# Optimization experiments

Measured on AMD Instinct MI355X. Metric: run time of the kernel, lower is better.

Reference implementation:

```python
import jax, jax.numpy as jnp
import numpy as np

E = 1024   # embed_dim
H = 1024   # hidden_dim
NH = 16    # num_heads
HD = H // NH
B, P, C = 2, 1024, 1024


def _layernorm(x, g, b):
    m = jnp.mean(x, axis=-1, keepdims=True)
    v = jnp.mean((x - m) ** 2, axis=-1, keepdims=True)
    return (x - m) / jnp.sqrt(v + 1e-5) * g + b


def _attention(problem, context, Wq, bq, Wk, bk, Wv, bv, mask, num_heads, head_dim, head_out_dim):
    # Faithful to source: head axis LAST in the reshape, mask added AFTER softmax.
    batch = problem.shape[0]
    q = (problem @ Wq + bq).reshape(batch, -1, head_dim, num_heads)      # b i d h
    k = (context @ Wk + bk).reshape(batch, -1, head_dim, num_heads)      # b j d h
    v = (context @ Wv + bv).reshape(batch, -1, head_out_dim, num_heads)  # b j o h
    scores = jnp.einsum('bidh,bjdh->bijh', q, k) / jnp.sqrt(jnp.asarray(head_dim, q.dtype))
    p = jax.nn.softmax(scores, axis=2)
    if mask is not None:
        p = p + mask[..., None]
    out = jnp.einsum('bijh,bjoh->bioh', p, v)
    return out.reshape(batch, -1, head_out_dim * num_heads)


def setup_inputs() -> dict:
    key = jax.random.key(0)
    ks = jax.random.split(key, 20)
    s = 0.02
    inp = {
        'x': jax.random.normal(ks[0], (B, P, E), jnp.float32),
        'context': jax.random.normal(ks[1], (B, C, E), jnp.float32),
        'causal_mask': jnp.zeros((B, P, P), jnp.float32),
        'problem_pad_mask': jnp.zeros((B, P, P), jnp.float32),
        'context_pad_mask': jnp.zeros((B, P, C), jnp.float32),
        # self-attn params (out_dim = E)
        'sa_Wq': jax.random.normal(ks[2], (E, H), jnp.float32) * s, 'sa_bq': jnp.zeros((H,), jnp.float32),
        'sa_Wk': jax.random.normal(ks[3], (E, H), jnp.float32) * s, 'sa_bk': jnp.zeros((H,), jnp.float32),
        'sa_Wv': jax.random.normal(ks[4], (E, E), jnp.float32) * s, 'sa_bv': jnp.zeros((E,), jnp.float32),
        # cross-attn params
        'ca_Wq': jax.random.normal(ks[5], (E, H), jnp.float32) * s, 'ca_bq': jnp.zeros((H,), jnp.float32),
        'ca_Wk': jax.random.normal(ks[6], (E, H), jnp.float32) * s, 'ca_bk': jnp.zeros((H,), jnp.float32),
        'ca_Wv': jax.random.normal(ks[7], (E, E), jnp.float32) * s, 'ca_bv': jnp.zeros((E,), jnp.float32),
        # layernorms
        'ln1_g': jnp.ones((E,), jnp.float32), 'ln1_b': jnp.zeros((E,), jnp.float32),
        'ln2_g': jnp.ones((E,), jnp.float32), 'ln2_b': jnp.zeros((E,), jnp.float32),
        'ln3_g': jnp.ones((E,), jnp.float32), 'ln3_b': jnp.zeros((E,), jnp.float32),
        # mlp
        'mlp_W1': jax.random.normal(ks[8], (E, H), jnp.float32) * s, 'mlp_b1': jnp.zeros((H,), jnp.float32),
        'mlp_W2': jax.random.normal(ks[9], (H, E), jnp.float32) * s, 'mlp_b2': jnp.zeros((E,), jnp.float32),
    }
    return inp


def reference(x, context, causal_mask, problem_pad_mask, context_pad_mask,
              sa_Wq, sa_bq, sa_Wk, sa_bk, sa_Wv, sa_bv,
              ca_Wq, ca_bq, ca_Wk, ca_bk, ca_Wv, ca_bv,
              ln1_g, ln1_b, ln2_g, ln2_b, ln3_g, ln3_b,
              mlp_W1, mlp_b1, mlp_W2, mlp_b2):
    self_attn_mask = causal_mask + problem_pad_mask
    xc = x
    x = _attention(x, x, sa_Wq, sa_bq, sa_Wk, sa_bk, sa_Wv, sa_bv, self_attn_mask, NH, HD, E // NH)
    x = _layernorm(x, ln1_g, ln1_b) + xc
    xc = x
    x = _attention(x, context, ca_Wq, ca_bq, ca_Wk, ca_bk, ca_Wv, ca_bv, context_pad_mask, NH, HD, E // NH)
    x = _layernorm(x, ln2_g, ln2_b) + xc
    xc = x
    x = jax.nn.relu(x @ mlp_W1 + mlp_b1) @ mlp_W2 + mlp_b2
    return _layernorm(x, ln3_g, ln3_b) + xc
```

## Files before the change

### kernel.cpp

```cpp
#include <hip/hip_runtime.h>
#include <math.h>

#define NHEADS 16

typedef __attribute__((ext_vector_type(8))) short bf16x8;
typedef __attribute__((ext_vector_type(4))) float f32x4;

__device__ inline short f2b(float f) {
  unsigned u = __float_as_uint(f);
  u += 0x7fffu + ((u >> 16) & 1u);
  return (short)(u >> 16);
}
__device__ inline float b2f(short s) {
  return __uint_as_float(((unsigned)(unsigned short)s) << 16);
}
__device__ inline void gld16(const void* g, void* l) {
  __builtin_amdgcn_global_load_lds(
      (const __attribute__((address_space(1))) unsigned int*)g,
      (__attribute__((address_space(3))) unsigned int*)l, 16, 0, 0);
}
#define MFMA16(a, b, c) __builtin_amdgcn_mfma_f32_16x16x32_bf16(a, b, c, 0, 0, 0)

__global__ __launch_bounds__(256) void prep_all(
    const float* __restrict__ x, const float* __restrict__ ctx,
    const float* __restrict__ cm, const float* __restrict__ ppm,
    const float* __restrict__ cpm,
    const float* sabq, const float* sabk, const float* sabv,
    const float* cabk, const float* cabv, const float* cabq,
    short* __restrict__ XB, short* __restrict__ CTXB,
    short* __restrict__ MBSA, short* __restrict__ MBCA,
    float* __restrict__ qkvb, float* __restrict__ kvb,
    float* __restrict__ qpb, unsigned* __restrict__ kmaxu) {
  const int blk = blockIdx.x;
  const int t = threadIdx.x;
  const int n4 = 2048 * 1024 / 4;
  if (blk < 8192) {
    int seg = blk >> 11;
    int i = (blk & 2047) * 256 + t;
    if (i >= n4) return;
    float4 va;
    short* out;
    if (seg == 0) { va = ((const float4*)x)[i]; out = XB; }
    else if (seg == 1) { va = ((const float4*)ctx)[i]; out = CTXB; }
    else if (seg == 2) {
      va = ((const float4*)cm)[i];
      float4 vb = ((const float4*)ppm)[i];
      va.x += vb.x; va.y += vb.y; va.z += vb.z; va.w += vb.w;
      out = MBSA;
    } else { va = ((const float4*)cpm)[i]; out = MBCA; }
    short4 s;
    s.x = f2b(va.x); s.y = f2b(va.y); s.z = f2b(va.z); s.w = f2b(va.w);
    ((short4*)out)[i] = s;
  } else {
    if (blk == 8192 && t < 64) kmaxu[t] = 0u;
    int i = (blk - 8192) * 256 + t;
    if (i >= 6144) return;
    int j = i & 1023;
    int pj = ((j & 63) << 4) | (j >> 6);
    int sec = i >> 10;
    if (sec == 0) qkvb[j] = sabq[pj];
    else if (sec == 1) qkvb[1024 + j] = sabk[pj];
    else if (sec == 2) qkvb[2048 + j] = sabv[pj];
    else if (sec == 3) kvb[j] = cabk[pj];
    else if (sec == 4) kvb[1024 + j] = cabv[pj];
    else qpb[j] = cabq[pj];
  }
}

__global__ __launch_bounds__(256) void wtrans(
    const float* W0, const float* W1, const float* W2, const float* W3,
    const float* W4, const float* W5, const float* W6, const float* W7,
    short* __restrict__ out) {
  __shared__ float t[64][65];
  const float* W;
  switch (blockIdx.z) {
    case 0: W = W0; break; case 1: W = W1; break;
    case 2: W = W2; break; case 3: W = W3; break;
    case 4: W = W4; break; case 5: W = W5; break;
    case 6: W = W6; break; default: W = W7; break;
  }
  const int permute = (blockIdx.z < 6) ? 1 : 0;
  short* o = out + (size_t)blockIdx.z * 1024 * 1024;
  const int tid = threadIdx.x;
  const int n0 = blockIdx.x * 64, k0 = blockIdx.y * 64;
  const int cg = (tid & 15) * 4, rg = tid >> 4;
  #pragma unroll
  for (int r = 0; r < 4; ++r) {
    int kl = rg + r * 16;
    float4 v = *(const float4*)(W + (size_t)(k0 + kl) * 1024 + n0 + cg);
    t[kl][cg + 0] = v.x; t[kl][cg + 1] = v.y;
    t[kl][cg + 2] = v.z; t[kl][cg + 3] = v.w;
  }
  __syncthreads();
  #pragma unroll
  for (int r = 0; r < 4; ++r) {
    int nl = rg + r * 16;
    int n = n0 + nl;
    int nrow = permute ? (((n & 15) << 6) | (n >> 4)) : n;
    short4 s;
    s.x = f2b(t[cg + 0][nl]); s.y = f2b(t[cg + 1][nl]);
    s.z = f2b(t[cg + 2][nl]); s.w = f2b(t[cg + 3][nl]);
    *(short4*)(o + (size_t)nrow * 1024 + k0 + cg) = s;
  }
}

__global__ __launch_bounds__(256) void knorm(const short* __restrict__ kh,
                                             unsigned* __restrict__ kmax) {
  const int bh = blockIdx.x, part = blockIdx.y;
  const int tid = threadIdx.x;
  const short* base = kh + (size_t)bh * 65536 +
                      (size_t)(part * 128 + (tid >> 1)) * 64 + (tid & 1) * 32;
  const bf16x8* rp = (const bf16x8*)base;
  float ssq = 0.f;
  #pragma unroll
  for (int c = 0; c < 4; ++c) {
    bf16x8 v = rp[c];
    #pragma unroll
    for (int e = 0; e < 8; ++e) { float f = b2f(v[e]); ssq += f * f; }
  }
  ssq += __shfl_xor(ssq, 1, 64);
  float mx = ssq;
  #pragma unroll
  for (int off = 2; off < 64; off <<= 1) mx = fmaxf(mx, __shfl_xor(mx, off, 64));
  __shared__ float wm[4];
  if ((tid & 63) == 0) wm[tid >> 6] = mx;
  __syncthreads();
  if (tid == 0)
    atomicMax(kmax + bh,
              __float_as_uint(fmaxf(fmaxf(wm[0], wm[1]), fmaxf(wm[2], wm[3]))));
}

__global__ __launch_bounds__(256) void gemm128(
    const short* __restrict__ A, const short* __restrict__ Bt,
    const float* __restrict__ bias,
    void* __restrict__ C0, short* __restrict__ C1, short* __restrict__ C2,
    int mode, int relu, int ny,
    const short* __restrict__ A2, const short* __restrict__ Bt2,
    const float* __restrict__ bias2,
    void* __restrict__ D0, short* __restrict__ D1, short* __restrict__ D2,
    int mode2, int relu2, int ny2) {
  if (blockIdx.z == 1) {
    A = A2; Bt = Bt2; bias = bias2;
    C0 = D0; C1 = D1; C2 = D2; mode = mode2; relu = relu2; ny = ny2;
  }
  if ((int)blockIdx.y >= ny) return;

  __shared__ short As[128 * 32];
  __shared__ short Bs[128 * 32];
  const int tid = threadIdx.x;
  const int w = tid >> 6, l = tid & 63;
  const int ln = l & 15, lq = l >> 4;
  const int wm = w >> 1, wn = w & 1;
  const int m0 = blockIdx.x * 128, n0 = blockIdx.y * 128;
  const int K = 1024;

  f32x4 acc[4][4];
  #pragma unroll
  for (int s = 0; s < 4; ++s)
    #pragma unroll
    for (int t = 0; t < 4; ++t) acc[s][t] = (f32x4){0.f, 0.f, 0.f, 0.f};

  const short* ga = A + (size_t)(m0 + w * 32 + (l >> 2)) * K + (l & 3) * 8;
  const short* gb = Bt + (size_t)(n0 + w * 32 + (l >> 2)) * K + (l & 3) * 8;
  short* lasA = &As[w * 1024];
  short* lasB = &Bs[w * 1024];

  for (int k0 = 0; k0 < K; k0 += 32) {
    __syncthreads();
    gld16(ga + k0, lasA);
    gld16(ga + (size_t)16 * K + k0, lasA + 512);
    gld16(gb + k0, lasB);
    gld16(gb + (size_t)16 * K + k0, lasB + 512);
    __syncthreads();
    bf16x8 af[4], bf[4];
    #pragma unroll
    for (int s = 0; s < 4; ++s)
      af[s] = *(const bf16x8*)&As[(wm * 64 + s * 16 + ln) * 32 + lq * 8];
    #pragma unroll
    for (int t = 0; t < 4; ++t)
      bf[t] = *(const bf16x8*)&Bs[(wn * 64 + t * 16 + ln) * 32 + lq * 8];
    #pragma unroll
    for (int s = 0; s < 4; ++s)
      #pragma unroll
      for (int t = 0; t < 4; ++t)
        acc[s][t] = MFMA16(af[s], bf[t], acc[s][t]);
  }

  float bv[4];
  #pragma unroll
  for (int t = 0; t < 4; ++t) bv[t] = bias[n0 + wn * 64 + t * 16 + ln];

  #pragma unroll
  for (int s = 0; s < 4; ++s) {
    #pragma unroll
    for (int t = 0; t < 4; ++t) {
      #pragma unroll
      for (int r = 0; r < 4; ++r) {
        int m = m0 + wm * 64 + s * 16 + lq * 4 + r;
        int n = n0 + wn * 64 + t * 16 + ln;
        float v = acc[s][t][r] + bv[t];
        if (relu) v = fmaxf(v, 0.f);
        int bb = m >> 10, ii = m & 1023;
        if (mode == 0) {
          ((float*)C0)[(size_t)m * 1024 + n] = v;
        } else if (mode == 1) {
          ((short*)C0)[(size_t)m * 1024 + n] = f2b(v);
        } else if (mode == 2) {
          int hh = n >> 6, d = n & 63;
          ((short*)C0)[(((size_t)(bb * 16 + hh)) * 1024 + ii) * 64 + d] = f2b(v);
        } else if (mode == 3) {
          int sel = n >> 10, g = n & 1023;
          int hh = g >> 6, d = g & 63;
          if (sel == 0)
            ((short*)C0)[(((size_t)(bb * 16 + hh)) * 1024 + ii) * 64 + d] = f2b(v);
          else if (sel == 1)
            C1[(((size_t)(bb * 16 + hh)) * 1024 + ii) * 64 + d] = f2b(v);
          else
            C2[(((size_t)(bb * 16 + hh)) * 64 + d) * 1024 + ii] = f2b(v);
        } else {
          int sel = n >> 10, g = n & 1023;
          int hh = g >> 6, d = g & 63;
          if (sel == 0)
            C1[(((size_t)(bb * 16 + hh)) * 1024 + ii) * 64 + d] = f2b(v);
          else
            C2[(((size_t)(bb * 16 + hh)) * 64 + d) * 1024 + ii] = f2b(v);
        }
      }
    }
  }
}

__global__ __launch_bounds__(256) void attn_flash(
    const short* __restrict__ qh, const short* __restrict__ kh,
    const short* __restrict__ vt, const short* __restrict__ maskb,
    const unsigned* __restrict__ kmax, float* __restrict__ out) {
  __shared__ short Ks[64 * 64];
  __shared__ short Vs[64 * 64];
  __shared__ short Msk[64 * 64];
  __shared__ short Ps[4][16 * 72];
  __shared__ float Ml[64];
  const int tid = threadIdx.x;
  const int w = tid >> 6, l = tid & 63;
  const int ln = l & 15, lq = l >> 4;
  const int it = blockIdx.x, h = blockIdx.y, b = blockIdx.z;
  const int i0 = it * 64;
  const int bh = b * 16 + h;
  const size_t bho = (size_t)bh * 65536;

  const short* qp = qh + bho + (size_t)(i0 + w * 16 + ln) * 64 + lq * 8;
  bf16x8 qf0 = *(const bf16x8*)qp;
  bf16x8 qf1 = *(const bf16x8*)(qp + 32);

  float ssq = 0.f;
  #pragma unroll
  for (int e = 0; e < 8; ++e) {
    float f0 = b2f(qf0[e]), f1 = b2f(qf1[e]);
    ssq += f0 * f0 + f1 * f1;
  }
  ssq += __shfl_xor(ssq, 16, 64);
  ssq += __shfl_xor(ssq, 32, 64);
  float km = sqrtf(__uint_as_float(kmax[bh])) * 1.0001f;
  if (lq == 0) Ml[w * 16 + ln] = sqrtf(ssq) * km * 0.125f + 1e-3f;
  float Mr[4], lac[4];
  #pragma unroll
  for (int r = 0; r < 4; ++r) { Mr[r] = Ml[w * 16 + lq * 4 + r]; lac[r] = 0.f; }

  const int srow = l >> 3;
  const int sch = (l & 7) ^ (srow & 7);
  const short* gk = kh + bho + (size_t)(w * 16 + srow) * 64 + sch * 8;
  const short* gv = vt + bho + (size_t)(w * 16 + srow) * 1024 + sch * 8;
  const short* gm = maskb + ((size_t)(b * 1024 + i0 + w * 16 + srow)) * 1024 + sch * 8;
  short* lk = &Ks[w * 1024];
  short* lv = &Vs[w * 1024];
  short* lm = &Msk[w * 1024];
  short* PsW = &Ps[w][0];

  f32x4 oa[4], mo[4];
  #pragma unroll
  for (int os = 0; os < 4; ++os) {
    oa[os] = (f32x4){0.f, 0.f, 0.f, 0.f};
    mo[os] = (f32x4){0.f, 0.f, 0.f, 0.f};
  }

  const int c0 = (lq ^ (ln & 7)) * 8;
  const int c1 = ((4 | lq) ^ (ln & 7)) * 8;

  for (int jt = 0; jt < 16; ++jt) {
    __syncthreads();
    gld16(gk + (size_t)jt * 4096, lk);
    gld16(gk + (size_t)jt * 4096 + 512, lk + 512);
    gld16(gv + (size_t)jt * 64, lv);
    gld16(gv + (size_t)jt * 64 + 8192, lv + 512);
    gld16(gm + (size_t)jt * 64, lm);
    gld16(gm + (size_t)jt * 64 + 8192, lm + 512);
    __syncthreads();

    f32x4 sa[4];
    #pragma unroll
    for (int js = 0; js < 4; ++js) {
      const short* kr = &Ks[(js * 16 + ln) * 64];
      bf16x8 kb0 = *(const bf16x8*)(kr + c0);
      bf16x8 kb1 = *(const bf16x8*)(kr + c1);
      f32x4 s = (f32x4){0.f, 0.f, 0.f, 0.f};
      s = MFMA16(qf0, kb0, s);
      s = MFMA16(qf1, kb1, s);
      sa[js] = s;
    }
    #pragma unroll
    for (int js = 0; js < 4; ++js)
      #pragma unroll
      for (int r = 0; r < 4; ++r) {
        float p = __expf(sa[js][r] * 0.125f - Mr[r]);
        lac[r] += p;
        PsW[(lq * 4 + r) * 72 + js * 16 + ln] = f2b(p);
      }
    bf16x8 pa0 = *(const bf16x8*)&PsW[ln * 72 + lq * 8];
    bf16x8 pa1 = *(const bf16x8*)&PsW[ln * 72 + 32 + lq * 8];
    const short* mr = &Msk[(w * 16 + ln) * 64];
    bf16x8 ma0 = *(const bf16x8*)(mr + c0);
    bf16x8 ma1 = *(const bf16x8*)(mr + c1);
    #pragma unroll
    for (int os = 0; os < 4; ++os) {
      const short* vr = &Vs[(os * 16 + ln) * 64];
      bf16x8 vb0 = *(const bf16x8*)(vr + c0);
      bf16x8 vb1 = *(const bf16x8*)(vr + c1);
      oa[os] = MFMA16(pa0, vb0, oa[os]);
      oa[os] = MFMA16(pa1, vb1, oa[os]);
      mo[os] = MFMA16(ma0, vb0, mo[os]);
      mo[os] = MFMA16(ma1, vb1, mo[os]);
    }
  }

  #pragma unroll
  for (int r = 0; r < 4; ++r) {
    lac[r] += __shfl_xor(lac[r], 1, 64);
    lac[r] += __shfl_xor(lac[r], 2, 64);
    lac[r] += __shfl_xor(lac[r], 4, 64);
    lac[r] += __shfl_xor(lac[r], 8, 64);
  }
  float inv[4];
  #pragma unroll
  for (int r = 0; r < 4; ++r) inv[r] = 1.f / lac[r];

  #pragma unroll
  for (int os = 0; os < 4; ++os)
    #pragma unroll
    for (int r = 0; r < 4; ++r) {
      int row = i0 + w * 16 + lq * 4 + r;
      int o = os * 16 + ln;
      out[bho + (size_t)row * 64 + o] = oa[os][r] * inv[r] + mo[os][r];
    }
}

__global__ __launch_bounds__(256) void ln_kernel(
    const float* __restrict__ x, const short* __restrict__ res,
    const float* __restrict__ g, const float* __restrict__ be,
    void* __restrict__ outp, int out_bf16, int inmode) {
  const int row = blockIdx.x;
  const int tid = threadIdx.x;
  float4 v;
  if (inmode == 0) {
    v = ((const float4*)(x + (size_t)row * 1024))[tid];
  } else {
    int b = row >> 10, i = row & 1023;
    const float* base = x + (size_t)b * 16 * 65536 + (size_t)i * 64;
    int o = tid >> 2, h0 = (tid & 3) * 4;
    v.x = base[(size_t)(h0 + 0) * 65536 + o];
    v.y = base[(size_t)(h0 + 1) * 65536 + o];
    v.z = base[(size_t)(h0 + 2) * 65536 + o];
    v.w = base[(size_t)(h0 + 3) * 65536 + o];
  }
  float s = v.x + v.y + v.z + v.w;
  float sq = v.x * v.x + v.y * v.y + v.z * v.z + v.w * v.w;
  #pragma unroll
  for (int off = 32; off > 0; off >>= 1) {
    s += __shfl_down(s, off, 64);
    sq += __shfl_down(sq, off, 64);
  }
  __shared__ float rs[4], rq[4], stat[2];
  int wave = tid >> 6, lane = tid & 63;
  if (lane == 0) { rs[wave] = s; rq[wave] = sq; }
  __syncthreads();
  if (tid == 0) {
    float S = rs[0] + rs[1] + rs[2] + rs[3];
    float Q = rq[0] + rq[1] + rq[2] + rq[3];
    float mean = S * (1.f / 1024.f);
    float var = Q * (1.f / 1024.f) - mean * mean;
    stat[0] = mean;
    stat[1] = rsqrtf(var + 1e-5f);
  }
  __syncthreads();
  float mean = stat[0], rstd = stat[1];
  float4 g4 = ((const float4*)g)[tid];
  float4 b4 = ((const float4*)be)[tid];
  short4 r4 = ((const short4*)(res + (size_t)row * 1024))[tid];
  float o0 = (v.x - mean) * rstd * g4.x + b4.x + b2f(r4.x);
  float o1 = (v.y - mean) * rstd * g4.y + b4.y + b2f(r4.y);
  float o2 = (v.z - mean) * rstd * g4.z + b4.z + b2f(r4.z);
  float o3 = (v.w - mean) * rstd * g4.w + b4.w + b2f(r4.w);
  if (out_bf16) {
    short4 o;
    o.x = f2b(o0); o.y = f2b(o1); o.z = f2b(o2); o.w = f2b(o3);
    ((short4*)outp)[(size_t)row * 256 + tid] = o;
  } else {
    float4 o = {o0, o1, o2, o3};
    ((float4*)outp)[(size_t)row * 256 + tid] = o;
  }
}

extern "C" void kernel_launch(void* const* d_in, const int* in_sizes, int n_in,
                              void* d_out, int out_size, void* d_ws, size_t ws_size,
                              hipStream_t stream) {
  const float* x    = (const float*)d_in[0];
  const float* ctx  = (const float*)d_in[1];
  const float* cm   = (const float*)d_in[2];
  const float* ppm  = (const float*)d_in[3];
  const float* cpm  = (const float*)d_in[4];
  const float* saWq = (const float*)d_in[5];
  const float* sabq = (const float*)d_in[6];
  const float* saWk = (const float*)d_in[7];
  const float* sabk = (const float*)d_in[8];
  const float* saWv = (const float*)d_in[9];
  const float* sabv = (const float*)d_in[10];
  const float* caWq = (const float*)d_in[11];
  const float* cabq = (const float*)d_in[12];
  const float* caWk = (const float*)d_in[13];
  const float* cabk = (const float*)d_in[14];
  const float* caWv = (const float*)d_in[15];
  const float* cabv = (const float*)d_in[16];
  const float* ln1g = (const float*)d_in[17];
  const float* ln1b = (const float*)d_in[18];
  const float* ln2g = (const float*)d_in[19];
  const float* ln2b = (const float*)d_in[20];
  const float* ln3g = (const float*)d_in[21];
  const float* ln3b = (const float*)d_in[22];
  const float* W1   = (const float*)d_in[23];
  const float* b1   = (const float*)d_in[24];
  const float* W2   = (const float*)d_in[25];
  const float* b2   = (const float*)d_in[26];

  char* ws = (char*)d_ws;
  const size_t MB = 1024 * 1024;
  short* WT       = (short*)(ws);
  float* qkvb     = (float*)(ws + 16 * MB);
  float* kvb      = (float*)(ws + 16 * MB + 16384);
  float* qpb      = (float*)(ws + 16 * MB + 32768);
  unsigned* kmaxu = (unsigned*)(ws + 16 * MB + 49152);
  short* MBSA  = (short*)(ws + 17 * MB);
  short* MBCA  = (short*)(ws + 21 * MB);
  short* XB    = (short*)(ws + 25 * MB);
  short* CTXB  = (short*)(ws + 29 * MB);
  short* QH    = (short*)(ws + 33 * MB);
  short* KH    = (short*)(ws + 37 * MB);
  short* VT    = (short*)(ws + 41 * MB);
  float* S3    = (float*)(ws + 45 * MB);
  short* X1B   = (short*)(ws + 53 * MB);
  short* X2B   = MBSA;
  short* HB    = CTXB;
  float* outp  = (float*)d_out;

  dim3 lg(2048);
  const short* dsp = nullptr;
  const float* dfp = nullptr;

  wtrans<<<dim3(16, 16, 8), 256, 0, stream>>>(saWq, saWk, saWv, caWk, caWv,
                                              caWq, W1, W2, WT);
  prep_all<<<dim3(8216), 256, 0, stream>>>(x, ctx, cm, ppm, cpm,
                                           sabq, sabk, sabv, cabk, cabv, cabq,
                                           XB, CTXB, MBSA, MBCA, qkvb, kvb, qpb,
                                           kmaxu);

  gemm128<<<dim3(16, 24, 1), 256, 0, stream>>>(
      XB, WT, qkvb, QH, KH, VT, 3, 0, 24,
      dsp, dsp, dfp, nullptr, nullptr, nullptr, 0, 0, 0);
  knorm<<<dim3(32, 8), 256, 0, stream>>>(KH, kmaxu);
  attn_flash<<<dim3(16, 16, 2), 256, 0, stream>>>(QH, KH, VT, MBSA, kmaxu, S3);
  ln_kernel<<<lg, 256, 0, stream>>>(S3, XB, ln1g, ln1b, X1B, 1, 1);

  gemm128<<<dim3(16, 16, 2), 256, 0, stream>>>(
      X1B, WT + 5 * 1048576, qpb, QH, nullptr, nullptr, 2, 0, 8,
      CTXB, WT + 3 * 1048576, kvb, nullptr, KH, VT, 4, 0, 16);
  knorm<<<dim3(32, 8), 256, 0, stream>>>(KH, kmaxu + 32);
  attn_flash<<<dim3(16, 16, 2), 256, 0, stream>>>(QH, KH, VT, MBCA, kmaxu + 32, S3);
  ln_kernel<<<lg, 256, 0, stream>>>(S3, X1B, ln2g, ln2b, X2B, 1, 1);

  gemm128<<<dim3(16, 8, 1), 256, 0, stream>>>(
      X2B, WT + 6 * 1048576, b1, HB, nullptr, nullptr, 1, 1, 8,
      dsp, dsp, dfp, nullptr, nullptr, nullptr, 0, 0, 0);
  gemm128<<<dim3(16, 8, 1), 256, 0, stream>>>(
      HB, WT + 7 * 1048576, b2, S3, nullptr, nullptr, 0, 0, 8,
      dsp, dsp, dfp, nullptr, nullptr, nullptr, 0, 0, 0);
  ln_kernel<<<lg, 256, 0, stream>>>(S3, X2B, ln3g, ln3b, outp, 0, 0);
}
```

Baseline: 350.0 us.

## Retile GEMMs to 64-row blocks with K=64 steps and XOR-swizzled LDS

Replaces the fixed 128x128 GEMM with a templated kernel that uses 64-row M tiles, a configurable N tile (128 or 64), and a K step of 64. LDS chunks are XOR-swizzled to avoid bank conflicts. Grids grow so that more blocks fill the CUs, since the old 16x8 grids used only 128 blocks for the MLP GEMMs. In exchange each block reuses less data, so global and LDS traffic per FLOP goes up.

```diff
diff --git a/kernel.cpp b/kernel.cpp
--- a/kernel.cpp
+++ b/kernel.cpp
@@ -130,7 +130,8 @@
               __float_as_uint(fmaxf(fmaxf(wm[0], wm[1]), fmaxf(wm[2], wm[3]))));
 }
 
-__global__ __launch_bounds__(256) void gemm128(
+template <int TN>
+__global__ __launch_bounds__(256) void gemmT(
     const short* __restrict__ A, const short* __restrict__ Bt,
     const float* __restrict__ bias,
     void* __restrict__ C0, short* __restrict__ C1, short* __restrict__ C2,
@@ -145,59 +146,67 @@
   }
   if ((int)blockIdx.y >= ny) return;
 
-  __shared__ short As[128 * 32];
-  __shared__ short Bs[128 * 32];
+  constexpr int NT = TN / 32;
+  constexpr int BR = TN / 4;
+  __shared__ short As[64 * 64];
+  __shared__ short Bs[TN * 64];
   const int tid = threadIdx.x;
   const int w = tid >> 6, l = tid & 63;
   const int ln = l & 15, lq = l >> 4;
   const int wm = w >> 1, wn = w & 1;
-  const int m0 = blockIdx.x * 128, n0 = blockIdx.y * 128;
+  const int m0 = blockIdx.x * 64, n0 = blockIdx.y * TN;
   const int K = 1024;
 
-  f32x4 acc[4][4];
-  #pragma unroll
-  for (int s = 0; s < 4; ++s)
-    #pragma unroll
-    for (int t = 0; t < 4; ++t) acc[s][t] = (f32x4){0.f, 0.f, 0.f, 0.f};
-
-  const short* ga = A + (size_t)(m0 + w * 32 + (l >> 2)) * K + (l & 3) * 8;
-  const short* gb = Bt + (size_t)(n0 + w * 32 + (l >> 2)) * K + (l & 3) * 8;
-  short* lasA = &As[w * 1024];
-  short* lasB = &Bs[w * 1024];
-
-  for (int k0 = 0; k0 < K; k0 += 32) {
+  f32x4 acc[2][NT];
+  #pragma unroll
+  for (int s = 0; s < 2; ++s)
+    #pragma unroll
+    for (int t = 0; t < NT; ++t) acc[s][t] = (f32x4){0.f, 0.f, 0.f, 0.f};
+
+  const int srow = l >> 3;
+  const int sch = (l & 7) ^ srow;
+  const short* ga = A + (size_t)(m0 + w * 16 + srow) * K + sch * 8;
+  const short* gb = Bt + (size_t)(n0 + w * BR + srow) * K + sch * 8;
+  short* la = &As[w * 16 * 64];
+  short* lb = &Bs[w * BR * 64];
+
+  for (int k0 = 0; k0 < K; k0 += 64) {
     __syncthreads();
-    gld16(ga + k0, lasA);
-    gld16(ga + (size_t)16 * K + k0, lasA + 512);
-    gld16(gb + k0, lasB);
-    gld16(gb + (size_t)16 * K + k0, lasB + 512);
+    gld16(ga + k0, la);
+    gld16(ga + (size_t)8 * K + k0, la + 512);
+    #pragma unroll
+    for (int rb = 0; rb < BR / 8; ++rb)
+      gld16(gb + (size_t)rb * 8 * K + k0, lb + rb * 512);
     __syncthreads();
-    bf16x8 af[4], bf[4];
-    #pragma unroll
-    for (int s = 0; s < 4; ++s)
-      af[s] = *(const bf16x8*)&As[(wm * 64 + s * 16 + ln) * 32 + lq * 8];
-    #pragma unroll
-    for (int t = 0; t < 4; ++t)
-      bf[t] = *(const bf16x8*)&Bs[(wn * 64 + t * 16 + ln) * 32 + lq * 8];
-    #pragma unroll
-    for (int s = 0; s < 4; ++s)
+    #pragma unroll
+    for (int kc = 0; kc < 2; ++kc) {
+      const int co = ((kc * 4 + lq) ^ (ln & 7)) * 8;
+      bf16x8 af[2], bf[NT];
+      af[0] = *(const bf16x8*)&As[(wm * 32 + ln) * 64 + co];
+      af[1] = *(const bf16x8*)&As[(wm * 32 + 16 + ln) * 64 + co];
       #pragma unroll
-      for (int t = 0; t < 4; ++t)
-        acc[s][t] = MFMA16(af[s], bf[t], acc[s][t]);
-  }
-
-  float bv[4];
-  #pragma unroll
-  for (int t = 0; t < 4; ++t) bv[t] = bias[n0 + wn * 64 + t * 16 + ln];
-
-  #pragma unroll
-  for (int s = 0; s < 4; ++s) {
-    #pragma unroll
-    for (int t = 0; t < 4; ++t) {
+      for (int t = 0; t < NT; ++t)
+        bf[t] = *(const bf16x8*)&Bs[(wn * (TN / 2) + t * 16 + ln) * 64 + co];
+      #pragma unroll
+      for (int s = 0; s < 2; ++s)
+        #pragma unroll
+        for (int t = 0; t < NT; ++t)
+          acc[s][t] = MFMA16(af[s], bf[t], acc[s][t]);
+    }
+  }
+
+  float bv[NT];
+  #pragma unroll
+  for (int t = 0; t < NT; ++t) bv[t] = bias[n0 + wn * (TN / 2) + t * 16 + ln];
+
+  #pragma unroll
+  for (int s = 0; s < 2; ++s) {
+    #pragma unroll
+    for (int t = 0; t < NT; ++t) {
       #pragma unroll
       for (int r = 0; r < 4; ++r) {
-        int m = m0 + wm * 64 + s * 16 + lq * 4 + r;
-        int n = n0 + wn * 64 + t * 16 + ln;
+        int m = m0 + wm * 32 + s * 16 + lq * 4 + r;
+        int n = n0 + wn * (TN / 2) + t * 16 + ln;
         float v = acc[s][t][r] + bv[t];
         if (relu) v = fmaxf(v, 0.f);
         int bb = m >> 10, ii = m & 1023;
@@ -470,25 +479,25 @@
                                            XB, CTXB, MBSA, MBCA, qkvb, kvb, qpb,
                                            kmaxu);
 
-  gemm128<<<dim3(16, 24, 1), 256, 0, stream>>>(
+  gemmT<128><<<dim3(32, 24, 1), 256, 0, stream>>>(
       XB, WT, qkvb, QH, KH, VT, 3, 0, 24,
       dsp, dsp, dfp, nullptr, nullptr, nullptr, 0, 0, 0);
   knorm<<<dim3(32, 8), 256, 0, stream>>>(KH, kmaxu);
   attn_flash<<<dim3(16, 16, 2), 256, 0, stream>>>(QH, KH, VT, MBSA, kmaxu, S3);
   ln_kernel<<<lg, 256, 0, stream>>>(S3, XB, ln1g, ln1b, X1B, 1, 1);
 
-  gemm128<<<dim3(16, 16, 2), 256, 0, stream>>>(
+  gemmT<128><<<dim3(32, 16, 2), 256, 0, stream>>>(
       X1B, WT + 5 * 1048576, qpb, QH, nullptr, nullptr, 2, 0, 8,
       CTXB, WT + 3 * 1048576, kvb, nullptr, KH, VT, 4, 0, 16);
   knorm<<<dim3(32, 8), 256, 0, stream>>>(KH, kmaxu + 32);
   attn_flash<<<dim3(16, 16, 2), 256, 0, stream>>>(QH, KH, VT, MBCA, kmaxu + 32, S3);
   ln_kernel<<<lg, 256, 0, stream>>>(S3, X1B, ln2g, ln2b, X2B, 1, 1);
 
-  gemm128<<<dim3(16, 8, 1), 256, 0, stream>>>(
-      X2B, WT + 6 * 1048576, b1, HB, nullptr, nullptr, 1, 1, 8,
+  gemmT<64><<<dim3(32, 16, 1), 256, 0, stream>>>(
+      X2B, WT + 6 * 1048576, b1, HB, nullptr, nullptr, 1, 1, 16,
       dsp, dsp, dfp, nullptr, nullptr, nullptr, 0, 0, 0);
-  gemm128<<<dim3(16, 8, 1), 256, 0, stream>>>(
-      HB, WT + 7 * 1048576, b2, S3, nullptr, nullptr, 0, 0, 8,
+  gemmT<64><<<dim3(32, 16, 1), 256, 0, stream>>>(
+      HB, WT + 7 * 1048576, b2, S3, nullptr, nullptr, 0, 0, 16,
       dsp, dsp, dfp, nullptr, nullptr, nullptr, 0, 0, 0);
   ln_kernel<<<lg, 256, 0, stream>>>(S3, X2B, ln3g, ln3b, outp, 0, 0);
 }
```

After: 299.0 us. 1.17x faster.
